# Kernel tuning notes

Hardware: AMD Instinct MI355X
Metric: run time of the kernel (lower is better)

## Reference

```python
import math
import jax, jax.numpy as jnp
import numpy as np

N_HEADS = 16
D_EMBED = 1024
D_HEAD = D_EMBED // N_HEADS


def setup_inputs() -> dict:
    key = jax.random.key(0)
    k1, k2, k3, k4, k5 = jax.random.split(key, 5)
    B, S, D = 4, 2048, D_EMBED
    scale = 1.0 / math.sqrt(D)
    return {
        "x": jax.random.normal(k1, (B, S, D), dtype=jnp.float32),
        "in_proj_w": jax.random.normal(k2, (3 * D, D), dtype=jnp.float32) * scale,
        "in_proj_b": jax.random.normal(k3, (3 * D,), dtype=jnp.float32) * 0.02,
        "out_proj_w": jax.random.normal(k4, (D, D), dtype=jnp.float32) * scale,
        "out_proj_b": jax.random.normal(k5, (D,), dtype=jnp.float32) * 0.02,
        "causal_mask": 0,
    }


def reference(x, in_proj_w, in_proj_b, out_proj_w, out_proj_b, causal_mask):
    B, S, D = x.shape
    # in_proj: torch Linear -> x @ W^T + b, then chunk into q,k,v
    qkv = x @ in_proj_w.T + in_proj_b              # [B,S,3D]
    q, k, v = jnp.split(qkv, 3, axis=-1)
    # [B,S,D] -> [B,H,S,d]
    def heads(t):
        return t.reshape(B, S, N_HEADS, D_HEAD).transpose(0, 2, 1, 3)
    q, k, v = heads(q), heads(k), heads(v)
    weight = jnp.einsum("bhsd,bhtd->bhst", q, k)   # [B,H,S,S] materialized scores
    if causal_mask:
        mask = jnp.triu(jnp.ones((S, S), dtype=bool), k=1)
        weight = jnp.where(mask, -jnp.inf, weight)
    weight = jax.nn.softmax(weight / math.sqrt(D_HEAD), axis=-1)
    out = jnp.einsum("bhst,bhtd->bhsd", weight, v)  # [B,H,S,d]
    out = out.transpose(0, 2, 1, 3).reshape(B, S, D)
    return out @ out_proj_w.T + out_proj_b
```

## Files before the change

kernel.cpp:

```cpp
#include <hip/hip_runtime.h>

typedef unsigned short u16;
typedef _Float16 h8 __attribute__((ext_vector_type(8)));
typedef __fp16 fp16x2 __attribute__((ext_vector_type(2)));
typedef float f32x4 __attribute__((ext_vector_type(4)));

constexpr int B_ = 4, S_ = 2048, D_ = 1024, H_ = 16;

__device__ __forceinline__ void async16(const void* g, void* l) {
  __builtin_amdgcn_global_load_lds(
      (const __attribute__((address_space(1))) void*)g,
      (__attribute__((address_space(3))) void*)l, 16, 0, 0);
}

__device__ __forceinline__ unsigned pk2(float a, float b) {
  union { fp16x2 h; unsigned u; } c;
  c.h = __builtin_amdgcn_cvt_pkrtz(a, b);
  return c.u;
}

__device__ __forceinline__ float fexp2(float x) {
#if __has_builtin(__builtin_amdgcn_exp2f)
  return __builtin_amdgcn_exp2f(x);
#else
  return exp2f(x);
#endif
}

#define QSCALE 0.18033688011112042f

__global__ __launch_bounds__(256) void cvt3_kernel(
    const float* __restrict__ x, const float* __restrict__ wi,
    const float* __restrict__ wo, _Float16* __restrict__ xh,
    _Float16* __restrict__ wih, _Float16* __restrict__ woh)
{
  const int bid = blockIdx.x;
  const float* src;
  _Float16* dst;
  int base;
  if (bid < 8192)       { src = x;  dst = xh;  base = bid; }
  else if (bid < 11264) { src = wi; dst = wih; base = bid - 8192; }
  else                  { src = wo; dst = woh; base = bid - 11264; }
  const int i = (base * 256 + threadIdx.x) * 4;
  const float4 v = *(const float4*)(src + i);
  uint2 o;
  o.x = pk2(v.x, v.y);
  o.y = pk2(v.z, v.w);
  *(uint2*)(dst + i) = o;
}

template<bool OUT_HALF, int BPW, bool SCALE_Q, bool FUSE_V>
__global__ __launch_bounds__(512, 2) void gemm256d_f16(
    const _Float16* __restrict__ A, const _Float16* __restrict__ Bw,
    const float* __restrict__ bias, void* __restrict__ Cout,
    _Float16* __restrict__ vTout,
    int M, int N, int K)
{
  constexpr int BN = BPW * 64;
  constexpr int NBB = BN / 8;
  __shared__ __align__(16) _Float16 sA[2][16384];
  __shared__ __align__(16) _Float16 sB[2][NBB * 512];

  const int tid = threadIdx.x;
  const int lane = tid & 63, w = tid >> 6;
  const int wm = w >> 2, wn = w & 3;

  const int id = blockIdx.x;
  const int cpx = gridDim.x >> 3;
  const int swz = (id & 7) * cpx + (id >> 3);
  const int nbx = N / BN;
  const int bx = swz % nbx, by = swz / nbx;
  const int m0 = by * 256, n0 = bx * BN;

  const int r15 = lane & 15, s4 = lane >> 4;
  const _Float16* gA[4];
  int loA[4];
#pragma unroll
  for (int j = 0; j < 4; ++j) {
    const int t = 2 * w + (j >> 1), kk = j & 1;
    gA[j] = A + (size_t)(m0 + 16 * t + r15) * K + kk * 32 + s4 * 8;
    loA[j] = (t * 2 + kk) * 512;
  }
  const _Float16* gB[BPW];
  int loB[BPW];
#pragma unroll
  for (int j = 0; j < BPW; ++j) {
    const int f = w * BPW + j, nt = f >> 1, kk = f & 1;
    gB[j] = Bw + (size_t)(n0 + 16 * nt + r15) * K + kk * 32 + s4 * 8;
    loB[j] = f * 512;
  }

  const f32x4 zf = {0.f, 0.f, 0.f, 0.f};
  f32x4 acc[8][BPW];
#pragma unroll
  for (int i = 0; i < 8; ++i)
#pragma unroll
    for (int j = 0; j < BPW; ++j) acc[i][j] = zf;

#pragma unroll
  for (int j = 0; j < 4; ++j) async16(gA[j], &sA[0][loA[j]]);
#pragma unroll
  for (int j = 0; j < BPW; ++j) async16(gB[j], &sB[0][loB[j]]);
#pragma unroll
  for (int j = 0; j < 4; ++j) async16(gA[j] + 64, &sA[1][loA[j]]);
#pragma unroll
  for (int j = 0; j < BPW; ++j) async16(gB[j] + 64, &sB[1][loB[j]]);
  if constexpr (BPW == 2)      asm volatile("s_waitcnt vmcnt(6)" ::: "memory");
  else if constexpr (BPW == 3) asm volatile("s_waitcnt vmcnt(7)" ::: "memory");
  else                         asm volatile("s_waitcnt vmcnt(8)" ::: "memory");
  __builtin_amdgcn_s_barrier();

  const int NT = K >> 6;
  int cur = 0;
  for (int kt = 0; kt < NT; ++kt) {
    const _Float16* pA = sA[cur];
    const _Float16* pB = sB[cur];
    _Float16* nA = sA[cur];
    _Float16* nB = sB[cur];
    const bool st = (kt + 2 < NT);
    const int ko = (kt + 2) * 64;

    h8 fb[BPW][2];
#pragma unroll
    for (int p = 0; p < 4; ++p) {
      if (p == 0) {
#pragma unroll
        for (int nt = 0; nt < BPW; ++nt)
#pragma unroll
          for (int kk = 0; kk < 2; ++kk)
            fb[nt][kk] = *(const h8*)&pB[((wn * BPW + nt) * 2 + kk) * 512 + lane * 8];
      } else if (st) {
        if (p == 1) {
#pragma unroll
          for (int j = 0; j < BPW; ++j) async16(gB[j] + ko, &nB[loB[j]]);
        }
        if ((w & 3) == p - 1) {
#pragma unroll
          for (int j = 0; j < 4; ++j) async16(gA[j] + ko, &nA[loA[j]]);
        }
      }
      h8 fa[2][2];
#pragma unroll
      for (int i = 0; i < 2; ++i)
#pragma unroll
        for (int kk = 0; kk < 2; ++kk)
          fa[i][kk] = *(const h8*)&pA[((wm * 8 + 2 * p + i) * 2 + kk) * 512 + lane * 8];
      __builtin_amdgcn_s_setprio(1);
#pragma unroll
      for (int i = 0; i < 2; ++i)
#pragma unroll
        for (int nt = 0; nt < BPW; ++nt)
#pragma unroll
          for (int kk = 0; kk < 2; ++kk)
            acc[2 * p + i][nt] = __builtin_amdgcn_mfma_f32_16x16x32_f16(
                fa[i][kk], fb[nt][kk], acc[2 * p + i][nt], 0, 0, 0);
      __builtin_amdgcn_s_setprio(0);
      __builtin_amdgcn_s_barrier();
    }
    if (st && (w & 3) == 3) {
#pragma unroll
      for (int j = 0; j < 4; ++j) async16(gA[j] + ko, &nA[loA[j]]);
    }
    if (kt + 1 < NT) {
      if (st) {
        if constexpr (BPW == 2)      asm volatile("s_waitcnt vmcnt(6)" ::: "memory");
        else if constexpr (BPW == 3) asm volatile("s_waitcnt vmcnt(7)" ::: "memory");
        else                         asm volatile("s_waitcnt vmcnt(8)" ::: "memory");
      } else {
        asm volatile("s_waitcnt vmcnt(0)" ::: "memory");
      }
      __builtin_amdgcn_s_barrier();
    }
    cur ^= 1;
  }

  const int g = lane >> 4, cc = lane & 15;
#pragma unroll
  for (int nt = 0; nt < BPW; ++nt) {
    const int col = n0 + wn * (16 * BPW) + nt * 16 + cc;
    const float bv = bias[col];
    float qs = 1.0f;
    if constexpr (SCALE_Q) qs = (col < 1024) ? QSCALE : 1.0f;
#pragma unroll
    for (int mt = 0; mt < 8; ++mt) {
      const int rowb = m0 + wm * 128 + mt * 16 + g * 4;
      float vv[4];
#pragma unroll
      for (int r = 0; r < 4; ++r) {
        vv[r] = acc[mt][nt][r] + bv;
        if constexpr (SCALE_Q) vv[r] *= qs;
      }
      bool vcol = false;
      if constexpr (FUSE_V) vcol = (col >= 2048);
      if (vcol) {
        union { _Float16 hx[4]; uint2 u; } pv;
#pragma unroll
        for (int r = 0; r < 4; ++r) pv.hx[r] = (_Float16)vv[r];
        *(uint2*)&vTout[((size_t)(((rowb >> 11) << 10) + (col - 2048)) << 11) + (rowb & 2047)] = pv.u;
      } else {
#pragma unroll
        for (int r = 0; r < 4; ++r) {
          if constexpr (OUT_HALF)
            ((_Float16*)Cout)[(size_t)(rowb + r) * N + col] = (_Float16)vv[r];
          else
            ((float*)Cout)[(size_t)(rowb + r) * N + col] = vv[r];
        }
      }
    }
  }
}

template<bool OUT_HALF>
__global__ __launch_bounds__(256) void gemm_f16(
    const _Float16* __restrict__ A, const _Float16* __restrict__ Bw,
    const float* __restrict__ bias, void* __restrict__ Cout,
    int M, int N, int K)
{
  __shared__ __align__(16) _Float16 sA[4096];
  __shared__ __align__(16) _Float16 sB[4096];

  const int tid = threadIdx.x;
  const int lane = tid & 63, w = tid >> 6;
  const int wm = w & 1, wn = w >> 1;
  const int m0 = blockIdx.y * 128, n0 = blockIdx.x * 128;

  const int sr = 16 * w + (lane & 15);
  const int ss = lane >> 4;
  const _Float16* gA1 = A + (size_t)(m0 + sr) * K + 8 * ss;
  const _Float16* gA2 = gA1 + (size_t)64 * K;
  const _Float16* gB1 = Bw + (size_t)(n0 + sr) * K + 8 * ss;
  const _Float16* gB2 = gB1 + (size_t)64 * K;
  _Float16* lA1 = &sA[w * 512];
  _Float16* lA2 = &sA[(w + 4) * 512];
  _Float16* lB1 = &sB[w * 512];
  _Float16* lB2 = &sB[(w + 4) * 512];

  const f32x4 zf = {0.f, 0.f, 0.f, 0.f};
  f32x4 acc[4][4];
#pragma unroll
  for (int i = 0; i < 4; ++i)
#pragma unroll
    for (int j = 0; j < 4; ++j) acc[i][j] = zf;

  for (int k0 = 0; k0 < K; k0 += 32) {
    __syncthreads();
    async16(gA1 + k0, lA1);
    async16(gA2 + k0, lA2);
    async16(gB1 + k0, lB1);
    async16(gB2 + k0, lB2);
    __syncthreads();

    h8 fa[4], fb[4];
#pragma unroll
    for (int i = 0; i < 4; ++i) {
      fa[i] = *(const h8*)&sA[((wm * 4 + i) << 9) + (lane << 3)];
      fb[i] = *(const h8*)&sB[((wn * 4 + i) << 9) + (lane << 3)];
    }
#pragma unroll
    for (int i = 0; i < 4; ++i)
#pragma unroll
      for (int j = 0; j < 4; ++j)
        acc[i][j] = __builtin_amdgcn_mfma_f32_16x16x32_f16(fa[i], fb[j], acc[i][j], 0, 0, 0);
  }

  const int g = lane >> 4, cc = lane & 15;
#pragma unroll
  for (int j = 0; j < 4; ++j) {
    const int col = n0 + (wn * 4 + j) * 16 + cc;
    const float bv = bias[col];
#pragma unroll
    for (int i = 0; i < 4; ++i) {
      const int rowb = m0 + (wm * 4 + i) * 16 + g * 4;
#pragma unroll
      for (int r = 0; r < 4; ++r) {
        const float v = acc[i][j][r] + bv;
        if constexpr (OUT_HALF)
          ((_Float16*)Cout)[(size_t)(rowb + r) * N + col] = (_Float16)v;
        else
          ((float*)Cout)[(size_t)(rowb + r) * N + col] = v;
      }
    }
  }
}

__global__ __launch_bounds__(256, 4) void attn_f16(
    const _Float16* __restrict__ qkv, const _Float16* __restrict__ vT,
    _Float16* __restrict__ attnO, const int* __restrict__ causal_ptr)
{
  __shared__ __align__(16) _Float16 sQP[9216];
  __shared__ __align__(16) _Float16 sK[4096];
  __shared__ __align__(16) _Float16 sV[4096];

  const int tid = threadIdx.x, lane = tid & 63, w = tid >> 6;
  const int q4 = lane >> 4, cc = lane & 15;
  const int id = blockIdx.x;
  const int swz = (id & 7) * 128 + (id >> 3);
  const int bh = swz >> 4, b = bh >> 4, h = bh & 15;
  const int q0 = (swz & 15) << 7;
  const int causal = causal_ptr[0];

  {
    const int rr = lane & 15, sc8 = lane >> 4;
#pragma unroll
    for (int tt = 0; tt < 2; ++tt) {
      const int t = 2 * w + tt;
#pragma unroll
      for (int sh = 0; sh < 2; ++sh) {
        const _Float16* g = qkv + (size_t)(b * S_ + q0 + 16 * t + rr) * 3072 + h * 64 + 8 * (4 * sh + sc8);
        async16(g, &sQP[t * 1024 + sh * 512]);
      }
    }
  }
  __syncthreads();

  h8 qf[2][2];
#pragma unroll
  for (int m = 0; m < 2; ++m)
#pragma unroll
    for (int kk = 0; kk < 2; ++kk)
      qf[m][kk] = *(const h8*)&sQP[((2 * w + m) << 10) + (kk << 9) + (lane << 3)];

  h8 ones;
#pragma unroll
  for (int i = 0; i < 8; ++i) ones[i] = (_Float16)1.0f;

  const _Float16* gK = qkv + (size_t)(b * S_ + 16 * w + (lane & 15)) * 3072 + 1024 + h * 64 + 8 * (lane >> 4);
  const _Float16* gV = vT + (size_t)(bh * 64 + 16 * w + (lane & 15)) * S_ + 8 * (lane >> 4);
  _Float16* lK0 = &sK[w * 1024];
  _Float16* lV0 = &sV[w * 1024];

  const int wp = w * 2304;

  const f32x4 zf = {0.f, 0.f, 0.f, 0.f};
  f32x4 oa[2][4], lac[2];
#pragma unroll
  for (int m = 0; m < 2; ++m) {
    lac[m] = zf;
#pragma unroll
    for (int nt = 0; nt < 4; ++nt) oa[m][nt] = zf;
  }

  for (int j0 = 0; j0 < S_; j0 += 64) {
    if (causal && j0 > q0 + 127) break;
    __syncthreads();
    async16(gK + (size_t)j0 * 3072, lK0);
    async16(gK + (size_t)j0 * 3072 + 32, lK0 + 512);
    async16(gV + j0, lV0);
    async16(gV + j0 + 32, lV0 + 512);
    __syncthreads();

    f32x4 sc[2][4];
    __builtin_amdgcn_s_setprio(1);
#pragma unroll
    for (int nt = 0; nt < 4; ++nt) {
      const h8 kf0 = *(const h8*)&sK[(nt << 10) + (lane << 3)];
      const h8 kf1 = *(const h8*)&sK[(nt << 10) + 512 + (lane << 3)];
#pragma unroll
      for (int m = 0; m < 2; ++m) {
        sc[m][nt] = __builtin_amdgcn_mfma_f32_16x16x32_f16(kf0, qf[m][0], zf, 0, 0, 0);
        sc[m][nt] = __builtin_amdgcn_mfma_f32_16x16x32_f16(kf1, qf[m][1], sc[m][nt], 0, 0, 0);
      }
    }
    __builtin_amdgcn_s_setprio(0);

    if (causal) {
#pragma unroll
      for (int m = 0; m < 2; ++m)
#pragma unroll
        for (int nt = 0; nt < 4; ++nt)
#pragma unroll
          for (int r = 0; r < 4; ++r)
            if ((j0 + nt * 16 + q4 * 4 + r) > (q0 + 32 * w + m * 16 + cc))
              sc[m][nt][r] = -1.0e30f;
    }

#pragma unroll
    for (int m = 0; m < 2; ++m)
#pragma unroll
      for (int nt = 0; nt < 4; ++nt) {
        uint2 pk;
        pk.x = pk2(fexp2(sc[m][nt][0]), fexp2(sc[m][nt][1]));
        pk.y = pk2(fexp2(sc[m][nt][2]), fexp2(sc[m][nt][3]));
        *(uint2*)&sQP[wp + (m * 16 + cc) * 72 + nt * 16 + q4 * 4] = pk;
      }

    asm volatile("s_waitcnt lgkmcnt(0)" ::: "memory");

    h8 pf[2][2];
#pragma unroll
    for (int m = 0; m < 2; ++m)
#pragma unroll
      for (int kk = 0; kk < 2; ++kk)
        pf[m][kk] = *(const h8*)&sQP[wp + (m * 16 + cc) * 72 + kk * 32 + q4 * 8];

    __builtin_amdgcn_s_setprio(1);
#pragma unroll
    for (int m = 0; m < 2; ++m) {
      lac[m] = __builtin_amdgcn_mfma_f32_16x16x32_f16(pf[m][0], ones, lac[m], 0, 0, 0);
      lac[m] = __builtin_amdgcn_mfma_f32_16x16x32_f16(pf[m][1], ones, lac[m], 0, 0, 0);
    }
#pragma unroll
    for (int nt = 0; nt < 4; ++nt) {
      const h8 vf0 = *(const h8*)&sV[(nt << 10) + (lane << 3)];
      const h8 vf1 = *(const h8*)&sV[(nt << 10) + 512 + (lane << 3)];
#pragma unroll
      for (int m = 0; m < 2; ++m) {
        oa[m][nt] = __builtin_amdgcn_mfma_f32_16x16x32_f16(pf[m][0], vf0, oa[m][nt], 0, 0, 0);
        oa[m][nt] = __builtin_amdgcn_mfma_f32_16x16x32_f16(pf[m][1], vf1, oa[m][nt], 0, 0, 0);
      }
    }
    __builtin_amdgcn_s_setprio(0);
  }

#pragma unroll
  for (int m = 0; m < 2; ++m) {
    float inv[4];
#pragma unroll
    for (int r = 0; r < 4; ++r) inv[r] = 1.0f / lac[m][r];
#pragma unroll
    for (int nt = 0; nt < 4; ++nt) {
      const int col = h * 64 + nt * 16 + cc;
#pragma unroll
      for (int r = 0; r < 4; ++r) {
        const int row = b * S_ + q0 + 32 * w + m * 16 + q4 * 4 + r;
        attnO[(size_t)row * D_ + col] = (_Float16)(oa[m][nt][r] * inv[r]);
      }
    }
  }
}

extern "C" void kernel_launch(void* const* d_in, const int* in_sizes, int n_in,
                              void* d_out, int out_size, void* d_ws, size_t ws_size,
                              hipStream_t stream)
{
  const float* x  = (const float*)d_in[0];
  const float* wi = (const float*)d_in[1];
  const float* bi = (const float*)d_in[2];
  const float* wo = (const float*)d_in[3];
  const float* bo = (const float*)d_in[4];
  const int* causal = (const int*)d_in[5];

  _Float16* xh   = (_Float16*)d_ws;
  _Float16* wih  = xh + 8388608;
  _Float16* woh  = wih + 3145728;
  _Float16* qkvb = woh + 1048576;
  _Float16* vT   = qkvb + 25165824;
  _Float16* attn = vT + 8388608;

  const int M = B_ * S_;

  cvt3_kernel<<<12288, 256, 0, stream>>>(x, wi, wo, xh, wih, woh);

  gemm256d_f16<true, 3, true, true><<<512, 512, 0, stream>>>(
      xh, wih, bi, qkvb, vT, M, 3 * D_, D_);

  attn_f16<<<1024, 256, 0, stream>>>(qkvb, vT, attn, causal);

  gemm_f16<false><<<dim3(8, 64), 256, 0, stream>>>(
      attn, woh, bo, d_out, M, D_, D_);
}
```

Baseline: 294.6 us.

## Restructure QKV GEMM mainloop into barrier-gated half-K phases with split staging

Rewrites the QKV projection GEMM, now fixed at a 256x192 tile, into four phases per 64-wide K step. Each phase loads four A fragments and issues twelve MFMAs, with barriers and explicit lgkm and vm waits around it. Global-to-LDS staging is split into two 32-wide K halves, so the kernel keeps only one tile of lookahead instead of two. The LDS layout is also changed to per-16-row blocks. The aim is tighter interleaving of loads and MFMAs with fewer register fragments in flight, at the cost of more barriers per K step and a shorter prefetch distance.

```diff
diff --git a/kernel.cpp b/kernel.cpp
--- a/kernel.cpp
+++ b/kernel.cpp
@@ -28,6 +28,9 @@
 }
 
 #define QSCALE 0.18033688011112042f
+
+#define LGKM0 asm volatile("s_waitcnt lgkmcnt(0)" ::: "memory")
+#define FENCE asm volatile("" ::: "memory")
 
 __global__ __launch_bounds__(256) void cvt3_kernel(
     const float* __restrict__ x, const float* __restrict__ wi,
@@ -49,135 +52,119 @@
   *(uint2*)(dst + i) = o;
 }
 
-template<bool OUT_HALF, int BPW, bool SCALE_Q, bool FUSE_V>
-__global__ __launch_bounds__(512, 2) void gemm256d_f16(
+template<bool SCALE_Q, bool FUSE_V>
+__global__ __launch_bounds__(512, 2) void gemm256m_f16(
     const _Float16* __restrict__ A, const _Float16* __restrict__ Bw,
-    const float* __restrict__ bias, void* __restrict__ Cout,
-    _Float16* __restrict__ vTout,
-    int M, int N, int K)
+    const float* __restrict__ bias, _Float16* __restrict__ Cout,
+    _Float16* __restrict__ vTout, int M, int N, int K)
 {
-  constexpr int BN = BPW * 64;
-  constexpr int NBB = BN / 8;
   __shared__ __align__(16) _Float16 sA[2][16384];
-  __shared__ __align__(16) _Float16 sB[2][NBB * 512];
+  __shared__ __align__(16) _Float16 sB[2][12288];
 
   const int tid = threadIdx.x;
   const int lane = tid & 63, w = tid >> 6;
   const int wm = w >> 2, wn = w & 3;
+  const bool wb2 = (w < 4);
 
   const int id = blockIdx.x;
   const int cpx = gridDim.x >> 3;
   const int swz = (id & 7) * cpx + (id >> 3);
-  const int nbx = N / BN;
+  const int nbx = N / 192;
   const int bx = swz % nbx, by = swz / nbx;
-  const int m0 = by * 256, n0 = bx * BN;
+  const int m0 = by * 256, n0 = bx * 192;
 
   const int r15 = lane & 15, s4 = lane >> 4;
-  const _Float16* gA[4];
-  int loA[4];
-#pragma unroll
-  for (int j = 0; j < 4; ++j) {
-    const int t = 2 * w + (j >> 1), kk = j & 1;
-    gA[j] = A + (size_t)(m0 + 16 * t + r15) * K + kk * 32 + s4 * 8;
-    loA[j] = (t * 2 + kk) * 512;
-  }
-  const _Float16* gB[BPW];
-  int loB[BPW];
-#pragma unroll
-  for (int j = 0; j < BPW; ++j) {
-    const int f = w * BPW + j, nt = f >> 1, kk = f & 1;
-    gB[j] = Bw + (size_t)(n0 + 16 * nt + r15) * K + kk * 32 + s4 * 8;
-    loB[j] = f * 512;
-  }
+  const _Float16* gA0 = A + (size_t)(m0 + 32 * w + r15) * K + s4 * 8;
+  const _Float16* gA1 = A + (size_t)(m0 + 32 * w + 16 + r15) * K + s4 * 8;
+  const _Float16* gB0 = Bw + (size_t)(n0 + 16 * w + r15) * K + s4 * 8;
+  const _Float16* gB1 = Bw + (size_t)(n0 + 128 + 16 * w + r15) * K + s4 * 8;
+  const int lA0 = 2 * w * 1024;
+  const int lA1 = (2 * w + 1) * 1024;
+  const int lB0 = w * 1024;
+  const int lB1 = (8 + w) * 1024;
+
+  auto stageK = [&](int tt, int kk, int q) {
+    const int ko = tt * 64 + kk * 32;
+    const int kq = kk * 512;
+    async16(gA0 + ko, &sA[q][lA0 + kq]);
+    async16(gA1 + ko, &sA[q][lA1 + kq]);
+    async16(gB0 + ko, &sB[q][lB0 + kq]);
+    if (wb2) async16(gB1 + ko, &sB[q][lB1 + kq]);
+  };
+
+#define VMN do { if (wb2) asm volatile("s_waitcnt vmcnt(4)" ::: "memory"); \
+                 else     asm volatile("s_waitcnt vmcnt(3)" ::: "memory"); } while (0)
+#define VMZ asm volatile("s_waitcnt vmcnt(0)" ::: "memory")
 
   const f32x4 zf = {0.f, 0.f, 0.f, 0.f};
-  f32x4 acc[8][BPW];
+  f32x4 acc[8][3];
 #pragma unroll
   for (int i = 0; i < 8; ++i)
 #pragma unroll
-    for (int j = 0; j < BPW; ++j) acc[i][j] = zf;
-
-#pragma unroll
-  for (int j = 0; j < 4; ++j) async16(gA[j], &sA[0][loA[j]]);
-#pragma unroll
-  for (int j = 0; j < BPW; ++j) async16(gB[j], &sB[0][loB[j]]);
-#pragma unroll
-  for (int j = 0; j < 4; ++j) async16(gA[j] + 64, &sA[1][loA[j]]);
-#pragma unroll
-  for (int j = 0; j < BPW; ++j) async16(gB[j] + 64, &sB[1][loB[j]]);
-  if constexpr (BPW == 2)      asm volatile("s_waitcnt vmcnt(6)" ::: "memory");
-  else if constexpr (BPW == 3) asm volatile("s_waitcnt vmcnt(7)" ::: "memory");
-  else                         asm volatile("s_waitcnt vmcnt(8)" ::: "memory");
+    for (int j = 0; j < 3; ++j) acc[i][j] = zf;
+
+  stageK(0, 0, 0);
+  stageK(0, 1, 0);
+  VMN;
   __builtin_amdgcn_s_barrier();
+  FENCE;
+
+#define PHASE(I0, KK, PRE, POST)                                             \
+  {                                                                          \
+    h8 fa[4];                                                                \
+    _Pragma("unroll")                                                        \
+    for (int i = 0; i < 4; ++i)                                              \
+      fa[i] = *(const h8*)&pA[(wm * 8 + (I0) + i) * 1024 + (KK)*512 + lane * 8]; \
+    PRE;                                                                     \
+    FENCE;                                                                   \
+    __builtin_amdgcn_s_barrier();                                            \
+    LGKM0;                                                                   \
+    __builtin_amdgcn_sched_barrier(0);                                       \
+    __builtin_amdgcn_s_setprio(1);                                           \
+    _Pragma("unroll")                                                        \
+    for (int i = 0; i < 4; ++i)                                              \
+      _Pragma("unroll")                                                      \
+      for (int j = 0; j < 3; ++j)                                            \
+        acc[(I0) + i][j] = __builtin_amdgcn_mfma_f32_16x16x32_f16(           \
+            fa[i], fb[j], acc[(I0) + i][j], 0, 0, 0);                        \
+    __builtin_amdgcn_s_setprio(0);                                           \
+    POST;                                                                    \
+    FENCE;                                                                   \
+    __builtin_amdgcn_s_barrier();                                            \
+    FENCE;                                                                   \
+  }
 
   const int NT = K >> 6;
-  int cur = 0;
-  for (int kt = 0; kt < NT; ++kt) {
+  for (int T = 0; T < NT; ++T) {
+    const int cur = T & 1, nxt = cur ^ 1;
+    const bool st = (T + 1 < NT);
     const _Float16* pA = sA[cur];
     const _Float16* pB = sB[cur];
-    _Float16* nA = sA[cur];
-    _Float16* nB = sB[cur];
-    const bool st = (kt + 2 < NT);
-    const int ko = (kt + 2) * 64;
-
-    h8 fb[BPW][2];
-#pragma unroll
-    for (int p = 0; p < 4; ++p) {
-      if (p == 0) {
-#pragma unroll
-        for (int nt = 0; nt < BPW; ++nt)
-#pragma unroll
-          for (int kk = 0; kk < 2; ++kk)
-            fb[nt][kk] = *(const h8*)&pB[((wn * BPW + nt) * 2 + kk) * 512 + lane * 8];
-      } else if (st) {
-        if (p == 1) {
-#pragma unroll
-          for (int j = 0; j < BPW; ++j) async16(gB[j] + ko, &nB[loB[j]]);
-        }
-        if ((w & 3) == p - 1) {
-#pragma unroll
-          for (int j = 0; j < 4; ++j) async16(gA[j] + ko, &nA[loA[j]]);
-        }
-      }
-      h8 fa[2][2];
-#pragma unroll
-      for (int i = 0; i < 2; ++i)
-#pragma unroll
-        for (int kk = 0; kk < 2; ++kk)
-          fa[i][kk] = *(const h8*)&pA[((wm * 8 + 2 * p + i) * 2 + kk) * 512 + lane * 8];
-      __builtin_amdgcn_s_setprio(1);
-#pragma unroll
-      for (int i = 0; i < 2; ++i)
-#pragma unroll
-        for (int nt = 0; nt < BPW; ++nt)
-#pragma unroll
-          for (int kk = 0; kk < 2; ++kk)
-            acc[2 * p + i][nt] = __builtin_amdgcn_mfma_f32_16x16x32_f16(
-                fa[i][kk], fb[nt][kk], acc[2 * p + i][nt], 0, 0, 0);
-      __builtin_amdgcn_s_setprio(0);
-      __builtin_amdgcn_s_barrier();
-    }
-    if (st && (w & 3) == 3) {
-#pragma unroll
-      for (int j = 0; j < 4; ++j) async16(gA[j] + ko, &nA[loA[j]]);
-    }
-    if (kt + 1 < NT) {
-      if (st) {
-        if constexpr (BPW == 2)      asm volatile("s_waitcnt vmcnt(6)" ::: "memory");
-        else if constexpr (BPW == 3) asm volatile("s_waitcnt vmcnt(7)" ::: "memory");
-        else                         asm volatile("s_waitcnt vmcnt(8)" ::: "memory");
-      } else {
-        asm volatile("s_waitcnt vmcnt(0)" ::: "memory");
-      }
-      __builtin_amdgcn_s_barrier();
-    }
-    cur ^= 1;
-  }
+
+    h8 fb[3];
+
+#pragma unroll
+    for (int j = 0; j < 3; ++j)
+      fb[j] = *(const h8*)&pB[(wn * 3 + j) * 1024 + lane * 8];
+    PHASE(0, 0, { if (st) stageK(T + 1, 0, nxt); }, {})
+
+    PHASE(4, 0, {}, { if (st) VMN; else VMZ; })
+
+#pragma unroll
+    for (int j = 0; j < 3; ++j)
+      fb[j] = *(const h8*)&pB[(wn * 3 + j) * 1024 + 512 + lane * 8];
+    PHASE(0, 1, { if (st) stageK(T + 1, 1, nxt); }, {})
+
+    PHASE(4, 1, {}, { if (st) VMN; else VMZ; })
+  }
+#undef PHASE
+#undef VMN
+#undef VMZ
 
   const int g = lane >> 4, cc = lane & 15;
 #pragma unroll
-  for (int nt = 0; nt < BPW; ++nt) {
-    const int col = n0 + wn * (16 * BPW) + nt * 16 + cc;
+  for (int nt = 0; nt < 3; ++nt) {
+    const int col = n0 + wn * 48 + nt * 16 + cc;
     const float bv = bias[col];
     float qs = 1.0f;
     if constexpr (SCALE_Q) qs = (col < 1024) ? QSCALE : 1.0f;
@@ -199,12 +186,8 @@
         *(uint2*)&vTout[((size_t)(((rowb >> 11) << 10) + (col - 2048)) << 11) + (rowb & 2047)] = pv.u;
       } else {
 #pragma unroll
-        for (int r = 0; r < 4; ++r) {
-          if constexpr (OUT_HALF)
-            ((_Float16*)Cout)[(size_t)(rowb + r) * N + col] = (_Float16)vv[r];
-          else
-            ((float*)Cout)[(size_t)(rowb + r) * N + col] = vv[r];
-        }
+        for (int r = 0; r < 4; ++r)
+          Cout[(size_t)(rowb + r) * N + col] = (_Float16)vv[r];
       }
     }
   }
@@ -384,7 +367,7 @@
         *(uint2*)&sQP[wp + (m * 16 + cc) * 72 + nt * 16 + q4 * 4] = pk;
       }
 
-    asm volatile("s_waitcnt lgkmcnt(0)" ::: "memory");
+    LGKM0;
 
     h8 pf[2][2];
 #pragma unroll
@@ -451,7 +434,7 @@
 
   cvt3_kernel<<<12288, 256, 0, stream>>>(x, wi, wo, xh, wih, woh);
 
-  gemm256d_f16<true, 3, true, true><<<512, 512, 0, stream>>>(
+  gemm256m_f16<true, true><<<512, 512, 0, stream>>>(
       xh, wih, bi, qkvb, vT, M, 3 * D_, D_);
 
   attn_f16<<<1024, 256, 0, stream>>>(qkvb, vT, attn, causal);
```

After: 295.0 us. Within noise of the previous version (+0.1%).
